# Kernel optimization log

Hardware: AMD Instinct MI355X
Metric: run time of the kernel (lower is better)

The kernel has to match this reference:

```python
import jax, jax.numpy as jnp
import numpy as np

# SS2D config: d_model=96, ssm_ratio=2 -> d_inner=192, d_state=16, dt_rank=ceil(96/16)=6, K=4
B_, H_, W_, DM = 4, 32, 32, 96
DI = 2 * DM          # d_inner = 192
N_STATE = 16
R_DT = 6
K = 4


def setup_inputs() -> dict:
    key = jax.random.key(0)
    ks = jax.random.split(key, 8)
    sc = lambda k, shape, s: jax.random.normal(k, shape, jnp.float32) * s
    A_logs = jnp.log(jnp.tile(jnp.arange(1, N_STATE + 1, dtype=jnp.float32)[None, :], (K * DI, 1)))
    return {
        "x": jax.random.normal(ks[0], (B_, H_, W_, DM), jnp.float32),
        "in_proj_w": sc(ks[1], (2 * DI, DM), 0.05),
        "conv_w": sc(ks[2], (DI, 1, 3, 3), 0.1),      # depthwise 3x3
        "conv_b": jnp.zeros((DI,), jnp.float32),
        "x_proj_weight": sc(ks[3], (K, R_DT + 2 * N_STATE, DI), 0.05),
        "dt_projs_weight": sc(ks[4], (K, DI, R_DT), 0.1),
        "dt_projs_bias": sc(ks[5], (K, DI), 0.1),
        "A_logs": A_logs,
        "Ds": jnp.ones((K * DI,), jnp.float32),
        "ln_gamma": jnp.ones((DI,), jnp.float32),
        "ln_beta": jnp.zeros((DI,), jnp.float32),
        "out_proj_w": sc(ks[6], (DM, DI), 0.05),
    }


def _selective_scan(xs, dts, As, Bs, Cs, Ds, delta_bias):
    # xs, dts: (B,K,D,L); As: (K,D,N); Bs, Cs: (B,K,N,L); Ds, delta_bias: (K,D)
    delta = jax.nn.softplus(dts + delta_bias[None, :, :, None])          # (B,K,D,L)
    dA = jnp.exp(jnp.einsum('bkdl,kdn->lbkdn', delta, As))               # (L,B,K,D,N)
    dBu = jnp.einsum('bkdl,bknl->lbkdn', delta * xs, Bs)                 # (L,B,K,D,N)

    def step(h, inp):
        dA_t, dBu_t = inp
        h = dA_t * h + dBu_t
        return h, h

    h0 = jnp.zeros(dA.shape[1:], dA.dtype)
    _, hs = jax.lax.scan(step, h0, (dA, dBu))                            # (L,B,K,D,N)
    ys = jnp.einsum('lbkdn,bknl->bkdl', hs, Cs)
    return ys + Ds[None, :, :, None] * xs


def reference(x, in_proj_w, conv_w, conv_b, x_proj_weight, dt_projs_weight,
              dt_projs_bias, A_logs, Ds, ln_gamma, ln_beta, out_proj_w):
    B, H, W, _ = x.shape
    L = H * W
    Rr = dt_projs_weight.shape[2]
    Nn = (x_proj_weight.shape[1] - Rr) // 2

    # in_proj -> split into ssm input and gate z
    xz = x @ in_proj_w.T                                                 # (B,H,W,2*DI)
    xi, z = jnp.split(xz, 2, axis=-1)

    # depthwise conv + SiLU
    xc = jnp.transpose(xi, (0, 3, 1, 2))                                 # (B,DI,H,W)
    Dch = xc.shape[1]
    xc = jax.lax.conv_general_dilated(
        xc, conv_w, window_strides=(1, 1), padding='SAME',
        feature_group_count=Dch,
        dimension_numbers=('NCHW', 'OIHW', 'NCHW')) + conv_b[None, :, None, None]
    xc = jax.nn.silu(xc)

    # 4-directional serialization: HW, WH, and their reverses
    x_flat = xc.reshape(B, Dch, L)
    x_t = jnp.transpose(xc, (0, 1, 3, 2)).reshape(B, Dch, L)
    x_hwwh = jnp.stack([x_flat, x_t], axis=1)                            # (B,2,D,L)
    xs = jnp.concatenate([x_hwwh, jnp.flip(x_hwwh, axis=-1)], axis=1)    # (B,4,D,L)

    x_dbl = jnp.einsum('bkdl,kcd->bkcl', xs, x_proj_weight)
    dts, Bs, Cs = jnp.split(x_dbl, [Rr, Rr + Nn], axis=2)
    dts = jnp.einsum('bkrl,kdr->bkdl', dts, dt_projs_weight)

    As = -jnp.exp(A_logs).reshape(4, Dch, Nn)
    Ds_ = Ds.reshape(4, Dch)
    out_y = _selective_scan(xs, dts, As, Bs, Cs, Ds_, dt_projs_bias)     # (B,4,D,L)

    inv_y = jnp.flip(out_y[:, 2:4], axis=-1)
    wh = lambda t: jnp.transpose(t.reshape(B, Dch, W, H), (0, 1, 3, 2)).reshape(B, Dch, L)
    y = out_y[:, 0] + inv_y[:, 0] + wh(out_y[:, 1]) + wh(inv_y[:, 1])
    y = jnp.transpose(y, (0, 2, 1)).reshape(B, H, W, Dch)

    # LayerNorm over channels
    mu = y.mean(-1, keepdims=True)
    var = ((y - mu) ** 2).mean(-1, keepdims=True)
    y = (y - mu) / jnp.sqrt(var + 1e-5) * ln_gamma + ln_beta

    y = y * jax.nn.silu(z)
    return y @ out_proj_w.T
```

## Files before the change

### kernel.cpp

```cpp
#include <hip/hip_runtime.h>
#include <hip/hip_bf16.h>
#include <hip/hip_fp16.h>

#define B_  4
#define H_  32
#define W_  32
#define DM  96
#define DI  192
#define NST 16
#define RDT 6
#define KD  4
#define L_  1024
#define C38 38

#define OFF_INW  0
#define OFF_CW   36864
#define OFF_CB   38592
#define OFF_XPW  38784
#define OFF_DTW  67968
#define OFF_DTB  72576
#define OFF_ALOG 73344
#define OFF_DS   85632
#define OFF_GAM  86400
#define OFF_BET  86592
#define OFF_OPW  86784
#define OFF_WT   105216
#define OFF_XPWT 142080
#define OFF_OPWT 171264
#define NCANON   189696

typedef __hip_bfloat16 bf16;

__device__ __forceinline__ float b2f(bf16 v) { return __bfloat162float(v); }
__device__ __forceinline__ float san(float v) { return fminf(fmaxf(v, -1.0e4f), 1.0e4f); }
__device__ __forceinline__ int lswap(int m) { return ((m & 31) << 5) | (m >> 5); }
__device__ __forceinline__ float ld_in(const void* p, int i, bool f32) {
    return f32 ? ((const float*)p)[i] : b2f(((const bf16*)p)[i]);
}

union H8 { float4 f4; __half2 h2[4]; };
__device__ __forceinline__ float h8get(const H8& v, int j) {
    return (j & 1) ? __high2float(v.h2[j >> 1]) : __low2float(v.h2[j >> 1]);
}
__device__ __forceinline__ void h8set(H8& v, int j, float f) {
    __half h = __float2half(f);
    if (j & 1) v.h2[j >> 1] = __halves2half2(__low2half(v.h2[j >> 1]), h);
    else       v.h2[j >> 1] = __halves2half2(h, __high2half(v.h2[j >> 1]));
}

__global__ void k_canon(const void* inw, const void* cw, const void* xpw,
                        const void* dtw, const void* alog, const void* opw,
                        const void* a768, const void* b768,
                        const void* a192, const void* b192, const void* c192,
                        float* __restrict__ wc) {
    int j = blockIdx.x * 256 + threadIdx.x;
    if (j > NCANON) return;
    unsigned wa = ((const unsigned*)a192)[0];
    unsigned wb = ((const unsigned*)b192)[0];
    bool f32;
    const void *gam, *cb, *bet;
    if (wa != 0u)      { gam = a192; cb = b192; bet = c192; f32 = (wa == 0x3F800000u); }
    else if (wb != 0u) { gam = b192; cb = a192; bet = c192; f32 = (wb == 0x3F800000u); }
    else               { gam = c192; cb = a192; bet = b192;
                         f32 = (((const unsigned*)c192)[0] == 0x3F800000u); }
    unsigned ones = f32 ? 0x3F800000u : 0x3F803F80u;
    const void *Ds, *dtb;
    if (((const unsigned*)a768)[0] == ones) { Ds = a768; dtb = b768; }
    else                                    { Ds = b768; dtb = a768; }

    if (j == NCANON) { wc[NCANON] = f32 ? 1.f : 0.f; return; }
    const void* p; int i;
    if      (j < OFF_CW)   { p = inw;  i = j - OFF_INW;  }
    else if (j < OFF_CB)   { p = cw;   i = j - OFF_CW;   }
    else if (j < OFF_XPW)  { p = cb;   i = j - OFF_CB;   }
    else if (j < OFF_DTW)  { p = xpw;  i = j - OFF_XPW;  }
    else if (j < OFF_DTB)  { p = dtw;  i = j - OFF_DTW;  }
    else if (j < OFF_ALOG) { p = dtb;  i = j - OFF_DTB;  }
    else if (j < OFF_DS)   { p = alog; i = j - OFF_ALOG; }
    else if (j < OFF_GAM)  { p = Ds;   i = j - OFF_DS;   }
    else if (j < OFF_BET)  { p = gam;  i = j - OFF_GAM;  }
    else if (j < OFF_OPW)  { p = bet;  i = j - OFF_BET;  }
    else if (j < OFF_WT)   { p = opw;  i = j - OFF_OPW;  }
    else if (j < OFF_XPWT) {
        int j2 = j - OFF_WT, m = j2 / (2 * DI), c = j2 % (2 * DI);
        p = inw; i = c * DM + m;
    }
    else if (j < OFF_OPWT) {
        int j2 = j - OFF_XPWT, kd = j2 / C38, c = j2 % C38;
        int k = kd / DI, d = kd % DI;
        p = xpw; i = (k * C38 + c) * DI + d;
    }
    else {
        int j2 = j - OFF_OPWT, dd = j2 / DM, tt = j2 % DM;
        p = opw; i = tt * DI + dd;
    }
    wc[j] = san(ld_in(p, i, f32));
}

__global__ void k_inproj(const void* __restrict__ x, const float* __restrict__ wc,
                         __half* __restrict__ xi, __half* __restrict__ gate) {
    __shared__ float xs[16][DM];
    int blk = blockIdx.x;
    int lt = blk & 63, b = blk >> 6;
    int l0 = lt * 16;
    int t = threadIdx.x;
    bool f32 = wc[NCANON] != 0.f;
    for (int idx = t; idx < 16 * DM; idx += 384) {
        int m = idx % DM, li = idx / DM;
        xs[li][m] = san(ld_in(x, (b * L_ + l0 + li) * DM + m, f32));
    }
    __syncthreads();

    const float* wt = wc + OFF_WT;
    float acc[16];
    #pragma unroll
    for (int j = 0; j < 16; ++j) acc[j] = 0.f;
    for (int m = 0; m < DM; ++m) {
        float wv = wt[m * (2 * DI) + t];
        #pragma unroll
        for (int j = 0; j < 16; ++j) acc[j] = fmaf(wv, xs[j][m], acc[j]);
    }

    if (t < DI) {
        H8 o0, o1;
        #pragma unroll
        for (int j = 0; j < 8; ++j) {
            h8set(o0, j, san(acc[j]));
            h8set(o1, j, san(acc[8 + j]));
        }
        float4* dst = (float4*)(xi + (b * DI + t) * L_ + l0);
        dst[0] = o0.f4;
        dst[1] = o1.f4;
    } else {
        int c = t - DI;
        #pragma unroll
        for (int j = 0; j < 16; ++j) {
            float z = san(acc[j]);
            float g = z / (1.f + __expf(-z));
            gate[(b * L_ + l0 + j) * DI + c] = __float2half(g);
        }
    }
}

__global__ void k_conv(const __half* __restrict__ xi, const float* __restrict__ wc,
                       __half* __restrict__ xc, __half* __restrict__ xcT) {
    __shared__ __half xin[L_];
    __shared__ __half xtr[33 * 32];
    int blk = blockIdx.x;
    int d = blk % DI, b = blk / DI;
    int t = threadIdx.x;
    const __half* src = xi + (b * DI + d) * L_;
    ((float2*)xin)[t] = ((const float2*)src)[t];
    float wgt[9];
    #pragma unroll
    for (int i = 0; i < 9; ++i) wgt[i] = wc[OFF_CW + d * 9 + i];
    float bias = wc[OFF_CB + d];
    __syncthreads();

    __half* dstN = xc  + (b * DI + d) * L_;
    #pragma unroll
    for (int r = 0; r < 4; ++r) {
        int l = r * 256 + t;
        int h = l >> 5, w = l & 31;
        float acc = bias;
        #pragma unroll
        for (int ky = 0; ky < 3; ++ky) {
            int hh = h + ky - 1;
            if (hh < 0 || hh >= H_) continue;
            #pragma unroll
            for (int kx = 0; kx < 3; ++kx) {
                int ww = w + kx - 1;
                if (ww < 0 || ww >= W_) continue;
                acc += __half2float(xin[hh * 32 + ww]) * wgt[ky * 3 + kx];
            }
        }
        acc = san(acc);
        __half v = __float2half(acc / (1.f + __expf(-acc)));
        dstN[l] = v;
        xtr[w * 33 + h] = v;
    }
    __syncthreads();
    __half* dstT = xcT + (b * DI + d) * L_;
    for (int i = t; i < L_; i += 256)
        dstT[i] = xtr[(i >> 5) * 33 + (i & 31)];
}

__global__ void k_proj(const __half* __restrict__ xc, const __half* __restrict__ xcT,
                       const float* __restrict__ wc, __half* __restrict__ xdbl) {
    __shared__ float xs_t[16][DI + 1];
    int blk = blockIdx.x;
    int lt = blk & 63, k = (blk >> 6) & 3, b = blk >> 8;
    int l0 = lt * 16;
    int t = threadIdx.x;
    int bk = b * KD + k;

    const __half* base = ((k & 1) ? xcT : xc) + b * DI * L_;
    for (int i = t; i < 16 * DI; i += 256) {
        int li = i & 15, d = i >> 4;
        int l = l0 + li;
        int src = (k < 2) ? l : (L_ - 1 - l);
        xs_t[li][d] = __half2float(base[d * L_ + src]);
    }
    __syncthreads();

    const float* xpwt = wc + OFF_XPWT + k * DI * C38;
    for (int o = t; o < 16 * C38; o += 256) {
        int li = o / C38, c = o % C38;
        float acc = 0.f;
        for (int d = 0; d < DI; ++d) acc += xpwt[d * C38 + c] * xs_t[li][d];
        xdbl[(bk * C38 + c) * L_ + l0 + li] = __float2half(san(acc));
    }
}

__global__ void k_scan(const __half* __restrict__ xdbl, const __half* __restrict__ xc,
                       const __half* __restrict__ xcTg, const float* __restrict__ wc,
                       __half* __restrict__ yb) {
    __shared__ __half xcN[L_], xcT[L_];
    __shared__ float  ybuf[KD][L_];
    int blk = blockIdx.x;
    int d = blk % DI, b = blk / DI;
    int t = threadIdx.x;
    for (int i = t; i < L_; i += 256) {
        xcN[i] = xc  [(b * DI + d) * L_ + i];
        xcT[i] = xcTg[(b * DI + d) * L_ + i];
    }

    int k = t >> 6, lane = t & 63;
    int bk = b * KD + k;
    int kd = k * DI + d;
    int l0 = lane * 16;

    float bias = wc[OFF_DTB + kd];
    float wv[RDT];
    #pragma unroll
    for (int r = 0; r < RDT; ++r) wv[r] = wc[OFF_DTW + kd * RDT + r];
    bool fast = true;
    #pragma unroll
    for (int n = 0; n < NST; ++n) {
        float An = -__expf(fminf(wc[OFF_ALOG + kd * NST + n], 30.f));
        if (fabsf(An + (float)(n + 1)) > 1e-3f * (float)(n + 1)) fast = false;
    }

    const __half* xd = xdbl + bk * C38 * L_;
    __syncthreads();

    float de[16];
    #pragma unroll
    for (int j = 0; j < 16; ++j) de[j] = bias;
    #pragma unroll
    for (int r = 0; r < RDT; ++r) {
        H8 v0, v1;
        v0.f4 = *(const float4*)(xd + r * L_ + l0);
        v1.f4 = *(const float4*)(xd + r * L_ + l0 + 8);
        #pragma unroll
        for (int j = 0; j < 8; ++j) {
            de[j]     += wv[r] * h8get(v0, j);
            de[8 + j] += wv[r] * h8get(v1, j);
        }
    }
    float dlt[16], du[16], e[16];
    #pragma unroll
    for (int j = 0; j < 16; ++j) {
        float dl = (de[j] > 20.f) ? de[j] : __logf(1.f + __expf(de[j]));
        dlt[j] = dl;
        int l = l0 + j;
        float u;
        if      (k == 0) u = __half2float(xcN[l]);
        else if (k == 1) u = __half2float(xcT[l]);
        else if (k == 2) u = __half2float(xcN[L_ - 1 - l]);
        else             u = __half2float(xcT[L_ - 1 - l]);
        du[j] = dl * u;
        e[j]  = __expf(-dl);
    }
    float P = 1.f;
    #pragma unroll
    for (int j = 0; j < 16; ++j) P *= e[j];

    float ecur[16];
    #pragma unroll
    for (int j = 0; j < 16; ++j) ecur[j] = e[j];
    float APn = P;
    float y[16];
    #pragma unroll
    for (int j = 0; j < 16; ++j) y[j] = 0.f;

    for (int n = 0; n < NST; ++n) {
        float A;
        if (fast) {
            A = APn;
        } else {
            float An = -__expf(fminf(wc[OFF_ALOG + kd * NST + n], 30.f));
            A = 1.f;
            #pragma unroll
            for (int j = 0; j < 16; ++j) { ecur[j] = __expf(dlt[j] * An); A *= ecur[j]; }
        }
        H8 bv0, bv1, cv0, cv1;
        bv0.f4 = *(const float4*)(xd + (RDT + n) * L_ + l0);
        bv1.f4 = *(const float4*)(xd + (RDT + n) * L_ + l0 + 8);
        cv0.f4 = *(const float4*)(xd + (RDT + NST + n) * L_ + l0);
        cv1.f4 = *(const float4*)(xd + (RDT + NST + n) * L_ + l0 + 8);
        float dub[16];
        #pragma unroll
        for (int j = 0; j < 8; ++j) {
            dub[j]     = du[j]     * h8get(bv0, j);
            dub[8 + j] = du[8 + j] * h8get(bv1, j);
        }
        float hloc = 0.f;
        #pragma unroll
        for (int j = 0; j < 16; ++j) hloc = fmaf(ecur[j], hloc, dub[j]);
        float aa = A, bb = hloc;
        #pragma unroll
        for (int off = 1; off < 64; off <<= 1) {
            float ap = __shfl_up(aa, off);
            float bp = __shfl_up(bb, off);
            bool ok = lane >= off;
            bb = ok ? fmaf(aa, bp, bb) : bb;
            aa = ok ? aa * ap : aa;
        }
        float carry = __shfl_up(bb, 1);
        if (lane == 0) carry = 0.f;
        float hh = carry;
        #pragma unroll
        for (int j = 0; j < 16; ++j) {
            hh = fmaf(ecur[j], hh, dub[j]);
            float Cn = (j < 8) ? h8get(cv0, j) : h8get(cv1, j - 8);
            y[j] = fmaf(Cn, hh, y[j]);
        }
        if (fast) {
            APn *= P;
            #pragma unroll
            for (int j = 0; j < 16; ++j) ecur[j] *= e[j];
        }
    }
    #pragma unroll
    for (int j = 0; j < 16; ++j) {
        int l = l0 + j;
        int idx = (k < 2) ? l : (L_ - 1 - l);
        ybuf[k][idx] = y[j];
    }
    __syncthreads();
    for (int i = t; i < L_; i += 256) {
        float v = ybuf[0][i] + ybuf[2][i]
                + ybuf[1][lswap(i)] + ybuf[3][lswap(i)];
        yb[(b * DI + d) * L_ + i] = __float2half(san(v));
    }
}

__global__ void k_merge(const __half* __restrict__ yb, const __half* __restrict__ xc,
                        const __half* __restrict__ gate, const float* __restrict__ wc,
                        float* __restrict__ out) {
    __shared__ float  yd[DI][17];
    __shared__ __half gt[16][DI + 8];
    __shared__ float  red[2][16][16];
    __shared__ float  yg[DI][17];
    __shared__ float  outt[16][DM + 1];
    int blk = blockIdx.x;
    int lt = blk & 63, b = blk >> 6;
    int l0 = lt * 16;
    int tid = threadIdx.x;
    int li = tid & 15, tq = tid >> 4;

    for (int idx = tid; idx < 16 * DI; idx += 256) {
        int l = idx / DI, c = idx % DI;
        gt[l][c] = gate[(b * L_ + l0 + l) * DI + c];
    }
    for (int idx = tid; idx < DI * 16; idx += 256) {
        int d = idx >> 4, l = idx & 15;
        float sD = wc[OFF_DS + d] + wc[OFF_DS + DI + d]
                 + wc[OFF_DS + 2 * DI + d] + wc[OFF_DS + 3 * DI + d];
        float v = __half2float(yb[(b * DI + d) * L_ + l0 + l])
                + sD * __half2float(xc[(b * DI + d) * L_ + l0 + l]);
        yd[d][l] = san(v);
    }
    __syncthreads();

    float s1 = 0.f, s2 = 0.f;
    #pragma unroll
    for (int j = 0; j < 12; ++j) {
        float v = yd[tq * 12 + j][li];
        s1 += v; s2 += v * v;
    }
    red[0][tq][li] = s1; red[1][tq][li] = s2;
    __syncthreads();
    float t1 = 0.f, t2 = 0.f;
    #pragma unroll
    for (int q = 0; q < 16; ++q) { t1 += red[0][q][li]; t2 += red[1][q][li]; }
    float mu  = t1 / DI;
    float var = t2 / DI - mu * mu;
    float inv = rsqrtf(fmaxf(var, 0.f) + 1e-5f);
    #pragma unroll
    for (int j = 0; j < 12; ++j) {
        int d = tq * 12 + j;
        float yn = (yd[d][li] - mu) * inv * wc[OFF_GAM + d] + wc[OFF_BET + d];
        yg[d][li] = yn * __half2float(gt[li][d]);
    }
    __syncthreads();

    float acc[6] = {0.f, 0.f, 0.f, 0.f, 0.f, 0.f};
    for (int dd = 0; dd < DI; ++dd) {
        float yv = yg[dd][li];
        const float* wp_ = wc + OFF_OPWT + dd * DM + tq * 6;
        #pragma unroll
        for (int j = 0; j < 6; ++j) acc[j] += wp_[j] * yv;
    }
    #pragma unroll
    for (int j = 0; j < 6; ++j) outt[li][tq * 6 + j] = san(acc[j]);
    __syncthreads();
    for (int idx = tid; idx < 16 * DM; idx += 256) {
        int l = idx / DM, tm = idx % DM;
        out[(b * L_ + l0 + l) * DM + tm] = outt[l][tm];
    }
}

extern "C" void kernel_launch(void* const* d_in, const int* in_sizes, int n_in,
                              void* d_out, int out_size, void* d_ws, size_t ws_size,
                              hipStream_t stream) {
    const void *x = 0, *inw = 0, *cw = 0, *xpw = 0, *dtw = 0, *alog = 0, *opw = 0;
    const void *p768[2] = {0, 0}, *p192[3] = {0, 0, 0};
    int n768 = 0, n192 = 0;
    for (int i = 0; i < n_in; ++i) {
        switch (in_sizes[i]) {
            case 393216: x    = d_in[i]; break;
            case 36864:  inw  = d_in[i]; break;
            case 1728:   cw   = d_in[i]; break;
            case 29184:  xpw  = d_in[i]; break;
            case 4608:   dtw  = d_in[i]; break;
            case 12288:  alog = d_in[i]; break;
            case 18432:  opw  = d_in[i]; break;
            case 768:    if (n768 < 2) p768[n768++] = d_in[i]; break;
            case 192:    if (n192 < 3) p192[n192++] = d_in[i]; break;
            default: break;
        }
    }

    float* out = (float*)d_out;

    float*  wcp   = (float*)d_ws;
    __half* bufA  = (__half*)(wcp + 189760);
    __half* xcp   = bufA + B_ * DI * L_;
    __half* xcTp  = xcp  + B_ * DI * L_;
    __half* ybp   = xcTp + B_ * DI * L_;
    __half* gatep = ybp  + B_ * DI * L_;

    k_canon <<<(NCANON + 1 + 255) / 256, 256, 0, stream>>>(
        inw, cw, xpw, dtw, alog, opw,
        p768[0], p768[1], p192[0], p192[1], p192[2], wcp);
    k_inproj<<<B_ * (L_ / 16), 384, 0, stream>>>(x, wcp, bufA, gatep);
    k_conv  <<<B_ * DI, 256, 0, stream>>>(bufA, wcp, xcp, xcTp);
    k_proj  <<<B_ * KD * (L_ / 16), 256, 0, stream>>>(xcp, xcTp, wcp, bufA);
    k_scan  <<<B_ * DI, 256, 0, stream>>>(bufA, xcp, xcTp, wcp, ybp);
    k_merge <<<B_ * (L_ / 16), 256, 0, stream>>>(ybp, xcp, gatep, wcp, out);
}
```

Baseline: 184.4 us.

## Batch scan shuffles across eight states and halve in_proj tile size

In the scan kernel's fast path, the per-state wavefront prefix scan is restructured so eight states are processed together. Their shuffle chains are interleaved to expose instruction-level parallelism and hide shuffle latency. This costs more registers and reloads B values in a second pass, which may reduce occupancy. Separately, in_proj uses 8-row tiles instead of 16, doubling the grid to improve occupancy at the cost of more weight reads.

```diff
diff --git a/kernel.cpp b/kernel.cpp
--- a/kernel.cpp
+++ b/kernel.cpp
@@ -99,42 +99,37 @@
 
 __global__ void k_inproj(const void* __restrict__ x, const float* __restrict__ wc,
                          __half* __restrict__ xi, __half* __restrict__ gate) {
-    __shared__ float xs[16][DM];
+    __shared__ float xs[8][DM];
     int blk = blockIdx.x;
-    int lt = blk & 63, b = blk >> 6;
-    int l0 = lt * 16;
+    int lt = blk & 127, b = blk >> 7;
+    int l0 = lt * 8;
     int t = threadIdx.x;
     bool f32 = wc[NCANON] != 0.f;
-    for (int idx = t; idx < 16 * DM; idx += 384) {
+    for (int idx = t; idx < 8 * DM; idx += 384) {
         int m = idx % DM, li = idx / DM;
         xs[li][m] = san(ld_in(x, (b * L_ + l0 + li) * DM + m, f32));
     }
     __syncthreads();
 
     const float* wt = wc + OFF_WT;
-    float acc[16];
-    #pragma unroll
-    for (int j = 0; j < 16; ++j) acc[j] = 0.f;
+    float acc[8];
+    #pragma unroll
+    for (int j = 0; j < 8; ++j) acc[j] = 0.f;
     for (int m = 0; m < DM; ++m) {
         float wv = wt[m * (2 * DI) + t];
         #pragma unroll
-        for (int j = 0; j < 16; ++j) acc[j] = fmaf(wv, xs[j][m], acc[j]);
+        for (int j = 0; j < 8; ++j) acc[j] = fmaf(wv, xs[j][m], acc[j]);
     }
 
     if (t < DI) {
-        H8 o0, o1;
-        #pragma unroll
-        for (int j = 0; j < 8; ++j) {
-            h8set(o0, j, san(acc[j]));
-            h8set(o1, j, san(acc[8 + j]));
-        }
-        float4* dst = (float4*)(xi + (b * DI + t) * L_ + l0);
-        dst[0] = o0.f4;
-        dst[1] = o1.f4;
+        H8 o0;
+        #pragma unroll
+        for (int j = 0; j < 8; ++j) h8set(o0, j, san(acc[j]));
+        *(float4*)(xi + (b * DI + t) * L_ + l0) = o0.f4;
     } else {
         int c = t - DI;
         #pragma unroll
-        for (int j = 0; j < 16; ++j) {
+        for (int j = 0; j < 8; ++j) {
             float z = san(acc[j]);
             float g = z / (1.f + __expf(-z));
             gate[(b * L_ + l0 + j) * DI + c] = __float2half(g);
@@ -157,7 +152,7 @@
     float bias = wc[OFF_CB + d];
     __syncthreads();
 
-    __half* dstN = xc  + (b * DI + d) * L_;
+    __half* dstN = xc + (b * DI + d) * L_;
     #pragma unroll
     for (int r = 0; r < 4; ++r) {
         int l = r * 256 + t;
@@ -258,11 +253,12 @@
             de[8 + j] += wv[r] * h8get(v1, j);
         }
     }
-    float dlt[16], du[16], e[16];
+    float du[16], e[16];
+    float dlt0[16];
     #pragma unroll
     for (int j = 0; j < 16; ++j) {
         float dl = (de[j] > 20.f) ? de[j] : __logf(1.f + __expf(de[j]));
-        dlt[j] = dl;
+        dlt0[j] = dl;
         int l = l0 + j;
         float u;
         if      (k == 0) u = __half2float(xcN[l]);
@@ -276,62 +272,122 @@
     #pragma unroll
     for (int j = 0; j < 16; ++j) P *= e[j];
 
-    float ecur[16];
-    #pragma unroll
-    for (int j = 0; j < 16; ++j) ecur[j] = e[j];
-    float APn = P;
     float y[16];
     #pragma unroll
     for (int j = 0; j < 16; ++j) y[j] = 0.f;
 
-    for (int n = 0; n < NST; ++n) {
-        float A;
-        if (fast) {
-            A = APn;
-        } else {
+    if (fast) {
+        float ecur[16];
+        #pragma unroll
+        for (int j = 0; j < 16; ++j) ecur[j] = e[j];
+        float APn = P;
+        #pragma unroll
+        for (int g = 0; g < 2; ++g) {
+            float aa[8], bb[8];
+            float ecg[16];
+            #pragma unroll
+            for (int j = 0; j < 16; ++j) ecg[j] = ecur[j];
+            #pragma unroll
+            for (int nn = 0; nn < 8; ++nn) {
+                int n = g * 8 + nn;
+                H8 bv0, bv1;
+                bv0.f4 = *(const float4*)(xd + (RDT + n) * L_ + l0);
+                bv1.f4 = *(const float4*)(xd + (RDT + n) * L_ + l0 + 8);
+                float hl = 0.f;
+                #pragma unroll
+                for (int j = 0; j < 8; ++j)  hl = fmaf(ecur[j],     hl, du[j]     * h8get(bv0, j));
+                #pragma unroll
+                for (int j = 0; j < 8; ++j)  hl = fmaf(ecur[8 + j], hl, du[8 + j] * h8get(bv1, j));
+                aa[nn] = APn; bb[nn] = hl;
+                APn *= P;
+                #pragma unroll
+                for (int j = 0; j < 16; ++j) ecur[j] *= e[j];
+            }
+            #pragma unroll
+            for (int off = 1; off < 64; off <<= 1) {
+                float ap[8], bp[8];
+                #pragma unroll
+                for (int nn = 0; nn < 8; ++nn) {
+                    ap[nn] = __shfl_up(aa[nn], off);
+                    bp[nn] = __shfl_up(bb[nn], off);
+                }
+                bool ok = lane >= off;
+                #pragma unroll
+                for (int nn = 0; nn < 8; ++nn) {
+                    bb[nn] = ok ? fmaf(aa[nn], bp[nn], bb[nn]) : bb[nn];
+                    aa[nn] = ok ? aa[nn] * ap[nn] : aa[nn];
+                }
+            }
+            float carry[8];
+            #pragma unroll
+            for (int nn = 0; nn < 8; ++nn) {
+                carry[nn] = __shfl_up(bb[nn], 1);
+                if (lane == 0) carry[nn] = 0.f;
+            }
+            #pragma unroll
+            for (int nn = 0; nn < 8; ++nn) {
+                int n = g * 8 + nn;
+                H8 bv0, bv1, cv0, cv1;
+                bv0.f4 = *(const float4*)(xd + (RDT + n) * L_ + l0);
+                bv1.f4 = *(const float4*)(xd + (RDT + n) * L_ + l0 + 8);
+                cv0.f4 = *(const float4*)(xd + (RDT + NST + n) * L_ + l0);
+                cv1.f4 = *(const float4*)(xd + (RDT + NST + n) * L_ + l0 + 8);
+                float hh = carry[nn];
+                #pragma unroll
+                for (int j = 0; j < 8; ++j) {
+                    hh = fmaf(ecg[j], hh, du[j] * h8get(bv0, j));
+                    y[j] = fmaf(h8get(cv0, j), hh, y[j]);
+                }
+                #pragma unroll
+                for (int j = 0; j < 8; ++j) {
+                    hh = fmaf(ecg[8 + j], hh, du[8 + j] * h8get(bv1, j));
+                    y[8 + j] = fmaf(h8get(cv1, j), hh, y[8 + j]);
+                }
+                #pragma unroll
+                for (int j = 0; j < 16; ++j) ecg[j] *= e[j];
+            }
+        }
+    } else {
+        for (int n = 0; n < NST; ++n) {
             float An = -__expf(fminf(wc[OFF_ALOG + kd * NST + n], 30.f));
-            A = 1.f;
-            #pragma unroll
-            for (int j = 0; j < 16; ++j) { ecur[j] = __expf(dlt[j] * An); A *= ecur[j]; }
+            float ec[16]; float A = 1.f;
+            #pragma unroll
+            for (int j = 0; j < 16; ++j) { ec[j] = __expf(dlt0[j] * An); A *= ec[j]; }
+            H8 bv0, bv1, cv0, cv1;
+            bv0.f4 = *(const float4*)(xd + (RDT + n) * L_ + l0);
+            bv1.f4 = *(const float4*)(xd + (RDT + n) * L_ + l0 + 8);
+            cv0.f4 = *(const float4*)(xd + (RDT + NST + n) * L_ + l0);
+            cv1.f4 = *(const float4*)(xd + (RDT + NST + n) * L_ + l0 + 8);
+            float dub[16];
+            #pragma unroll
+            for (int j = 0; j < 8; ++j) {
+                dub[j]     = du[j]     * h8get(bv0, j);
+                dub[8 + j] = du[8 + j] * h8get(bv1, j);
+            }
+            float hloc = 0.f;
+            #pragma unroll
+            for (int j = 0; j < 16; ++j) hloc = fmaf(ec[j], hloc, dub[j]);
+            float aa = A, bb = hloc;
+            #pragma unroll
+            for (int off = 1; off < 64; off <<= 1) {
+                float ap = __shfl_up(aa, off);
+                float bp = __shfl_up(bb, off);
+                bool ok = lane >= off;
+                bb = ok ? fmaf(aa, bp, bb) : bb;
+                aa = ok ? aa * ap : aa;
+            }
+            float carry = __shfl_up(bb, 1);
+            if (lane == 0) carry = 0.f;
+            float hh = carry;
+            #pragma unroll
+            for (int j = 0; j < 16; ++j) {
+                hh = fmaf(ec[j], hh, dub[j]);
+                float Cn = (j < 8) ? h8get(cv0, j) : h8get(cv1, j - 8);
+                y[j] = fmaf(Cn, hh, y[j]);
+            }
         }
-        H8 bv0, bv1, cv0, cv1;
-        bv0.f4 = *(const float4*)(xd + (RDT + n) * L_ + l0);
-        bv1.f4 = *(const float4*)(xd + (RDT + n) * L_ + l0 + 8);
-        cv0.f4 = *(const float4*)(xd + (RDT + NST + n) * L_ + l0);
-        cv1.f4 = *(const float4*)(xd + (RDT + NST + n) * L_ + l0 + 8);
-        float dub[16];
-        #pragma unroll
-        for (int j = 0; j < 8; ++j) {
-            dub[j]     = du[j]     * h8get(bv0, j);
-            dub[8 + j] = du[8 + j] * h8get(bv1, j);
-        }
-        float hloc = 0.f;
-        #pragma unroll
-        for (int j = 0; j < 16; ++j) hloc = fmaf(ecur[j], hloc, dub[j]);
-        float aa = A, bb = hloc;
-        #pragma unroll
-        for (int off = 1; off < 64; off <<= 1) {
-            float ap = __shfl_up(aa, off);
-            float bp = __shfl_up(bb, off);
-            bool ok = lane >= off;
-            bb = ok ? fmaf(aa, bp, bb) : bb;
-            aa = ok ? aa * ap : aa;
-        }
-        float carry = __shfl_up(bb, 1);
-        if (lane == 0) carry = 0.f;
-        float hh = carry;
-        #pragma unroll
-        for (int j = 0; j < 16; ++j) {
-            hh = fmaf(ecur[j], hh, dub[j]);
-            float Cn = (j < 8) ? h8get(cv0, j) : h8get(cv1, j - 8);
-            y[j] = fmaf(Cn, hh, y[j]);
-        }
-        if (fast) {
-            APn *= P;
-            #pragma unroll
-            for (int j = 0; j < 16; ++j) ecur[j] *= e[j];
-        }
-    }
+    }
+
     #pragma unroll
     for (int j = 0; j < 16; ++j) {
         int l = l0 + j;
@@ -445,7 +501,7 @@
     k_canon <<<(NCANON + 1 + 255) / 256, 256, 0, stream>>>(
         inw, cw, xpw, dtw, alog, opw,
         p768[0], p768[1], p192[0], p192[1], p192[2], wcp);
-    k_inproj<<<B_ * (L_ / 16), 384, 0, stream>>>(x, wcp, bufA, gatep);
+    k_inproj<<<B_ * (L_ / 8), 384, 0, stream>>>(x, wcp, bufA, gatep);
     k_conv  <<<B_ * DI, 256, 0, stream>>>(bufA, wcp, xcp, xcTp);
     k_proj  <<<B_ * KD * (L_ / 16), 256, 0, stream>>>(xcp, xcTp, wcp, bufA);
     k_scan  <<<B_ * DI, 256, 0, stream>>>(bufA, xcp, xcTp, wcp, ybp);
```

Result: slower. 378.9 us (+105.5%).
